# Kernel optimization log

Measured on AMD Instinct MI355X. Metric: run time of the kernel, lower is better.

Reference implementation:

```python
import jax, jax.numpy as jnp
import numpy as np

B, R, N, D_IN, D_OUT = 8, 8, 1024, 256, 256


def setup_inputs() -> dict:
    key = jax.random.key(0)
    k1, k2, k3, k4 = jax.random.split(key, 4)
    x = jax.random.normal(k1, (B, N, D_IN), dtype=jnp.float32)
    adj_stack = jax.random.uniform(k2, (B, R, N, N), dtype=jnp.float32)
    # per-relation Linear params, stacked: W[r] maps D_IN -> D_OUT
    bound = 1.0 / np.sqrt(D_IN)
    W = jax.random.uniform(k3, (R, D_IN, D_OUT), minval=-bound, maxval=bound, dtype=jnp.float32)
    b = jax.random.uniform(k4, (R, D_OUT), minval=-bound, maxval=bound, dtype=jnp.float32)
    return {"x": x, "adj_stack": adj_stack, "W": W, "b": b}


def reference(x, adj_stack, W, b):
    # support[b,r,n,e] = x[b,n,:] @ W[r] + b[r]
    support = jnp.einsum('bnd,rde->brne', x, W) + b[None, :, None, :]
    # out[b,m,e] = sum_r adj[b,r,m,:] @ support[b,r,:,e]
    out = jnp.einsum('brmn,brne->bme', adj_stack, support)
    return jax.nn.relu(out)
```

## Files before the change

### kernel.cpp

```cpp
#include <hip/hip_runtime.h>


#define Rr 8
#define Nn 1024
#define Dd 256
#define SP 104
#define EPF 68
#define EPS 72

typedef __attribute__((ext_vector_type(8))) short short8;
typedef __attribute__((ext_vector_type(4))) float f32x4;

__device__ __forceinline__ short f2bf(float f) {
    unsigned u = __builtin_bit_cast(unsigned, f);
    u += 0x7fffu + ((u >> 16) & 1u);
    return (short)(u >> 16);
}

__device__ __forceinline__ short8 cvt8(f32x4 lo, f32x4 hi) {
    short8 t;
    t[0] = f2bf(lo[0]); t[1] = f2bf(lo[1]); t[2] = f2bf(lo[2]); t[3] = f2bf(lo[3]);
    t[4] = f2bf(hi[0]); t[5] = f2bf(hi[1]); t[6] = f2bf(hi[2]); t[7] = f2bf(hi[3]);
    return t;
}

__global__ void prep_w_kernel(const float* __restrict__ W, short* __restrict__ Wt) {
    __shared__ short T[64][72];
    const int tid = threadIdx.x;
    const int et = blockIdx.x, dt = blockIdx.y, r = blockIdx.z;
    const float* Wr = W + ((size_t)r * Dd + dt * 64) * Dd + et * 64;
    #pragma unroll
    for (int i = 0; i < 4; ++i) {
        int idx = tid + i * 256;
        int d_l = idx >> 4;
        int e4  = (idx & 15) * 4;
        f32x4 v = *(const f32x4*)(Wr + d_l * Dd + e4);
        T[e4 + 0][d_l] = f2bf(v[0]);
        T[e4 + 1][d_l] = f2bf(v[1]);
        T[e4 + 2][d_l] = f2bf(v[2]);
        T[e4 + 3][d_l] = f2bf(v[3]);
    }
    __syncthreads();
    short* o = Wt + ((size_t)r * Dd + et * 64) * Dd + dt * 64;
    #pragma unroll
    for (int i = 0; i < 2; ++i) {
        int idx = tid + i * 256;
        *(short8*)(o + (idx >> 3) * Dd + (idx & 7) * 8) = *(const short8*)&T[idx >> 3][(idx & 7) * 8];
    }
}

__global__ __launch_bounds__(256, 3) void support_kernel(
        const float* __restrict__ x, const short* __restrict__ Wt,
        const float* __restrict__ bias, short* __restrict__ sup) {
    __shared__ short As[2][64 * SP];
    __shared__ short Bs[2][64 * SP];

    const int tid = threadIdx.x;
    const int wave = tid >> 6, lane = tid & 63;
    const int quad = lane >> 4, l16 = lane & 15;
    const int lrow = tid >> 3, lc = tid & 7;
    const int d = blockIdx.x;
    const int b = d & 7, rest = d >> 3;
    const int e_t = rest & 3, n_t = (rest >> 2) & 15, r = rest >> 6;
    const int e0 = e_t * 64, n0 = n_t * 64;
    const int we = wave & 1, wn = wave >> 1;

    const short* wp = Wt + ((size_t)r * Dd + e0) * Dd;
    const float* xb = x + ((size_t)b * Nn + n0) * Dd;

    short8 Wa0[2], Wa1[2];
    f32x4  Xv0[4], Xv1[4];

#define SGLOAD(WW, XX, t) do { int d0_ = (t) * 64;                              \
        _Pragma("unroll")                                                       \
        for (int p_ = 0; p_ < 2; ++p_) { int row_ = lrow + p_ * 32;             \
            WW[p_] = *(const short8*)(wp + (size_t)row_ * Dd + d0_ + lc * 8);   \
            const float* px_ = xb + (size_t)row_ * Dd + d0_ + lc * 8;           \
            XX[2 * p_]     = *(const f32x4*)px_;                                \
            XX[2 * p_ + 1] = *(const f32x4*)(px_ + 4); } } while (0)

#define SWRITE(BW, WW, XX) do {                                                 \
        _Pragma("unroll")                                                       \
        for (int p_ = 0; p_ < 2; ++p_) { int row_ = lrow + p_ * 32;             \
            *(short8*)&As[BW][row_ * SP + lc * 8] = WW[p_];                     \
            *(short8*)&Bs[BW][row_ * SP + lc * 8] = cvt8(XX[2 * p_], XX[2 * p_ + 1]); } } while (0)

#define SCOMP(BR) do {                                                          \
        _Pragma("unroll")                                                       \
        for (int kk_ = 0; kk_ < 2; ++kk_) { short8 af_[2], bf_[2];              \
            _Pragma("unroll")                                                   \
            for (int i_ = 0; i_ < 2; ++i_)                                      \
                af_[i_] = *(const short8*)&As[BR][(we * 32 + i_ * 16 + l16) * SP + kk_ * 32 + quad * 8]; \
            _Pragma("unroll")                                                   \
            for (int j_ = 0; j_ < 2; ++j_)                                      \
                bf_[j_] = *(const short8*)&Bs[BR][(wn * 32 + j_ * 16 + l16) * SP + kk_ * 32 + quad * 8]; \
            __builtin_amdgcn_s_setprio(1);                                      \
            _Pragma("unroll")                                                   \
            for (int i_ = 0; i_ < 2; ++i_)                                      \
                _Pragma("unroll")                                               \
                for (int j_ = 0; j_ < 2; ++j_)                                  \
                    acc[i_][j_] = __builtin_amdgcn_mfma_f32_16x16x32_bf16(af_[i_], bf_[j_], acc[i_][j_], 0, 0, 0); \
            __builtin_amdgcn_s_setprio(0); } } while (0)

#define SITER(t, VM, BW, WW, XX, BR) do {                                       \
        asm volatile("s_waitcnt vmcnt(" #VM ")" ::: "memory");                  \
        asm volatile("s_waitcnt lgkmcnt(0)" ::: "memory");                      \
        __builtin_amdgcn_s_barrier();                                           \
        asm volatile("" ::: "memory");                                          \
        SWRITE(BW, WW, XX);                                                     \
        if ((t) + 3 < 4) SGLOAD(WW, XX, (t) + 3);                               \
        SCOMP(BR); } while (0)

    f32x4 acc[2][2] = {};
    SGLOAD(Wa0, Xv0, 0);
    SGLOAD(Wa1, Xv1, 1);
    asm volatile("s_waitcnt vmcnt(6)" ::: "memory");
    SWRITE(0, Wa0, Xv0);
    SGLOAD(Wa0, Xv0, 2);
    SITER(0, 6, 1, Wa1, Xv1, 0);
    SITER(1, 6, 0, Wa0, Xv0, 1);
    SITER(2, 0, 1, Wa1, Xv1, 0);
    asm volatile("s_waitcnt lgkmcnt(0)" ::: "memory");
    __builtin_amdgcn_s_barrier();
    asm volatile("" ::: "memory");
    SCOMP(1);
#undef SGLOAD
#undef SWRITE
#undef SCOMP
#undef SITER

    __syncthreads();
    short* E = &As[0][0];
    #pragma unroll
    for (int i = 0; i < 2; ++i)
        #pragma unroll
        for (int reg = 0; reg < 4; ++reg) {
            int e_l = we * 32 + i * 16 + quad * 4 + reg;
            float bv = bias[r * Dd + e0 + e_l];
            #pragma unroll
            for (int j = 0; j < 2; ++j)
                E[e_l * EPS + wn * 32 + j * 16 + l16] = f2bf(acc[i][j][reg] + bv);
        }
    __syncthreads();
    #pragma unroll
    for (int p = 0; p < 2; ++p) {
        int idx = tid + p * 256;
        int row = idx >> 3, c = idx & 7;
        *(short8*)(sup + (((size_t)((b * Rr + r) * Dd + e0 + row)) << 10) + n0 + c * 8) =
            *(const short8*)&E[row * EPS + c * 8];
    }
}

__global__ __launch_bounds__(256, 3) void gcn_gemm_kernel(
        const float* __restrict__ adj, const short* __restrict__ sup,
        float* __restrict__ out) {
    __shared__ short As[2][64 * SP];
    __shared__ short Bs[2][64 * SP];

    const int tid = threadIdx.x;
    const int wave = tid >> 6, lane = tid & 63;
    const int quad = lane >> 4, l16 = lane & 15;
    const int lrow = tid >> 3, lc = tid & 7;
    const int d = blockIdx.x;
    const int L = (d & 7) * 64 + (d >> 3);
    const int e_t = L & 3, mrow = L >> 2;
    const int b = mrow >> 4;
    const int m0 = (mrow & 15) * 64, e0 = e_t * 64;
    const int wm = wave & 1, we = wave >> 1;

    f32x4  Aa0[4], Aa1[4];
    short8 Sv0[2], Sv1[2];

#define GGLOAD(AA, SS, t) do { int r_ = (t) >> 4, n0_ = ((t) & 15) * 64;        \
        const float* ap_ = adj + ((size_t)((b * Rr + r_) * Nn + m0)) * Nn + n0_; \
        const short* sp_ = sup + (((size_t)((b * Rr + r_) * Dd + e0)) << 10) + n0_; \
        _Pragma("unroll")                                                       \
        for (int p_ = 0; p_ < 2; ++p_) { int row_ = lrow + p_ * 32;             \
            const float* pa_ = ap_ + (size_t)row_ * Nn + lc * 8;                \
            AA[2 * p_]     = *(const f32x4*)pa_;                                \
            AA[2 * p_ + 1] = *(const f32x4*)(pa_ + 4);                          \
            SS[p_] = *(const short8*)(sp_ + ((size_t)row_ << 10) + lc * 8); } } while (0)

#define GWRITE(BW, AA, SS) do {                                                 \
        _Pragma("unroll")                                                       \
        for (int p_ = 0; p_ < 2; ++p_) { int row_ = lrow + p_ * 32;             \
            *(short8*)&As[BW][row_ * SP + lc * 8] = cvt8(AA[2 * p_], AA[2 * p_ + 1]); \
            *(short8*)&Bs[BW][row_ * SP + lc * 8] = SS[p_]; } } while (0)

#define GCOMP(BR) do {                                                          \
        _Pragma("unroll")                                                       \
        for (int kk_ = 0; kk_ < 2; ++kk_) { short8 af_[2], bf_[2];              \
            _Pragma("unroll")                                                   \
            for (int i_ = 0; i_ < 2; ++i_)                                      \
                af_[i_] = *(const short8*)&As[BR][(wm * 32 + i_ * 16 + l16) * SP + kk_ * 32 + quad * 8]; \
            _Pragma("unroll")                                                   \
            for (int j_ = 0; j_ < 2; ++j_)                                      \
                bf_[j_] = *(const short8*)&Bs[BR][(we * 32 + j_ * 16 + l16) * SP + kk_ * 32 + quad * 8]; \
            __builtin_amdgcn_s_setprio(1);                                      \
            _Pragma("unroll")                                                   \
            for (int i_ = 0; i_ < 2; ++i_)                                      \
                _Pragma("unroll")                                               \
                for (int j_ = 0; j_ < 2; ++j_)                                  \
                    acc[i_][j_] = __builtin_amdgcn_mfma_f32_16x16x32_bf16(af_[i_], bf_[j_], acc[i_][j_], 0, 0, 0); \
            __builtin_amdgcn_s_setprio(0); } } while (0)

#define GITER(t, VM, BW, AA, SS, BR) do {                                       \
        asm volatile("s_waitcnt vmcnt(" #VM ")" ::: "memory");                  \
        asm volatile("s_waitcnt lgkmcnt(0)" ::: "memory");                      \
        __builtin_amdgcn_s_barrier();                                           \
        asm volatile("" ::: "memory");                                          \
        GWRITE(BW, AA, SS);                                                     \
        if ((t) + 3 < 128) GGLOAD(AA, SS, (t) + 3);                             \
        GCOMP(BR); } while (0)

    f32x4 acc[2][2] = {};
    GGLOAD(Aa0, Sv0, 0);
    GGLOAD(Aa1, Sv1, 1);
    asm volatile("s_waitcnt vmcnt(6)" ::: "memory");
    GWRITE(0, Aa0, Sv0);
    GGLOAD(Aa0, Sv0, 2);
    for (int t = 0; t < 126; t += 2) {
        GITER(t,     6, 1, Aa1, Sv1, 0);
        GITER(t + 1, 6, 0, Aa0, Sv0, 1);
    }
    GITER(126, 0, 1, Aa1, Sv1, 0);
    asm volatile("s_waitcnt lgkmcnt(0)" ::: "memory");
    __builtin_amdgcn_s_barrier();
    asm volatile("" ::: "memory");
    GCOMP(1);
#undef GGLOAD
#undef GWRITE
#undef GCOMP
#undef GITER

    __syncthreads();
    float* E = (float*)&As[0][0];
    #pragma unroll
    for (int i = 0; i < 2; ++i)
        #pragma unroll
        for (int reg = 0; reg < 4; ++reg) {
            int m_l = wm * 32 + i * 16 + quad * 4 + reg;
            #pragma unroll
            for (int j = 0; j < 2; ++j)
                E[m_l * EPF + we * 32 + j * 16 + l16] = fmaxf(acc[i][j][reg], 0.f);
        }
    __syncthreads();
    #pragma unroll
    for (int p = 0; p < 4; ++p) {
        int idx = tid + p * 256;
        int row = idx >> 4, c = idx & 15;
        *(f32x4*)(out + ((size_t)(b * Nn + m0 + row)) * Dd + e0 + c * 4) =
            *(const f32x4*)&E[row * EPF + c * 4];
    }
}

extern "C" void kernel_launch(void* const* d_in, const int* in_sizes, int n_in,
                              void* d_out, int out_size, void* d_ws, size_t ws_size,
                              hipStream_t stream) {
    const float* x    = (const float*)d_in[0];
    const float* adj  = (const float*)d_in[1];
    const float* W    = (const float*)d_in[2];
    const float* bias = (const float*)d_in[3];
    float* out = (float*)d_out;
    short* sup = (short*)d_ws;
    short* Wt  = (short*)((char*)d_ws + (32u << 20));

    prep_w_kernel<<<dim3(4, 4, 8), 256, 0, stream>>>(W, Wt);
    support_kernel<<<4096, 256, 0, stream>>>(x, Wt, bias, sup);
    gcn_gemm_kernel<<<512, 256, 0, stream>>>(adj, sup, out);
}
```

Measured before the change: 442.3 us.

## Pre-pack support in MFMA fragment layout and load it directly into registers

The support kernel now writes its bf16 output in a packed layout that matches the MFMA B-operand fragment order, so the main GEMM loads B fragments straight from global memory into registers and skips LDS for them. The main GEMM tile changes from 64x64 to 32x128 (m by e), and only the adjacency tile is staged in LDS, through a 4-deep buffer with one barrier per iteration. This is meant to cut LDS traffic and barrier count in the bandwidth-bound adjacency stream. In exchange it holds more register buffers and issues uncoalesced-looking per-wave B loads from L2.

```diff
diff --git a/kernel.cpp b/kernel.cpp
--- a/kernel.cpp
+++ b/kernel.cpp
@@ -4,11 +4,12 @@
 #define Rr 8
 #define Nn 1024
 #define Dd 256
-#define SP 104
-#define EPF 68
+#define AP 104
+#define EP2 132
 #define EPS 72
 
 typedef __attribute__((ext_vector_type(8))) short short8;
+typedef __attribute__((ext_vector_type(4))) short short4s;
 typedef __attribute__((ext_vector_type(4))) float f32x4;
 
 __device__ __forceinline__ short f2bf(float f) {
@@ -21,6 +22,12 @@
     short8 t;
     t[0] = f2bf(lo[0]); t[1] = f2bf(lo[1]); t[2] = f2bf(lo[2]); t[3] = f2bf(lo[3]);
     t[4] = f2bf(hi[0]); t[5] = f2bf(hi[1]); t[6] = f2bf(hi[2]); t[7] = f2bf(hi[3]);
+    return t;
+}
+
+__device__ __forceinline__ short4s cvt4(f32x4 v) {
+    short4s t;
+    t[0] = f2bf(v[0]); t[1] = f2bf(v[1]); t[2] = f2bf(v[2]); t[3] = f2bf(v[3]);
     return t;
 }
 
@@ -51,9 +58,9 @@
 
 __global__ __launch_bounds__(256, 3) void support_kernel(
         const float* __restrict__ x, const short* __restrict__ Wt,
-        const float* __restrict__ bias, short* __restrict__ sup) {
-    __shared__ short As[2][64 * SP];
-    __shared__ short Bs[2][64 * SP];
+        const float* __restrict__ bias, short* __restrict__ supP) {
+    __shared__ short As[2][64 * AP];
+    __shared__ short Bs[2][64 * AP];
 
     const int tid = threadIdx.x;
     const int wave = tid >> 6, lane = tid & 63;
@@ -82,18 +89,18 @@
 #define SWRITE(BW, WW, XX) do {                                                 \
         _Pragma("unroll")                                                       \
         for (int p_ = 0; p_ < 2; ++p_) { int row_ = lrow + p_ * 32;             \
-            *(short8*)&As[BW][row_ * SP + lc * 8] = WW[p_];                     \
-            *(short8*)&Bs[BW][row_ * SP + lc * 8] = cvt8(XX[2 * p_], XX[2 * p_ + 1]); } } while (0)
+            *(short8*)&As[BW][row_ * AP + lc * 8] = WW[p_];                     \
+            *(short8*)&Bs[BW][row_ * AP + lc * 8] = cvt8(XX[2 * p_], XX[2 * p_ + 1]); } } while (0)
 
 #define SCOMP(BR) do {                                                          \
         _Pragma("unroll")                                                       \
         for (int kk_ = 0; kk_ < 2; ++kk_) { short8 af_[2], bf_[2];              \
             _Pragma("unroll")                                                   \
             for (int i_ = 0; i_ < 2; ++i_)                                      \
-                af_[i_] = *(const short8*)&As[BR][(we * 32 + i_ * 16 + l16) * SP + kk_ * 32 + quad * 8]; \
+                af_[i_] = *(const short8*)&As[BR][(we * 32 + i_ * 16 + l16) * AP + kk_ * 32 + quad * 8]; \
             _Pragma("unroll")                                                   \
             for (int j_ = 0; j_ < 2; ++j_)                                      \
-                bf_[j_] = *(const short8*)&Bs[BR][(wn * 32 + j_ * 16 + l16) * SP + kk_ * 32 + quad * 8]; \
+                bf_[j_] = *(const short8*)&Bs[BR][(wn * 32 + j_ * 16 + l16) * AP + kk_ * 32 + quad * 8]; \
             __builtin_amdgcn_s_setprio(1);                                      \
             _Pragma("unroll")                                                   \
             for (int i_ = 0; i_ < 2; ++i_)                                      \
@@ -144,113 +151,116 @@
     __syncthreads();
     #pragma unroll
     for (int p = 0; p < 2; ++p) {
-        int idx = tid + p * 256;
-        int row = idx >> 3, c = idx & 7;
-        *(short8*)(sup + (((size_t)((b * Rr + r) * Dd + e0 + row)) << 10) + n0 + c * 8) =
-            *(const short8*)&E[row * EPS + c * 8];
+        int chunk = tid + p * 256;
+        int e_l = chunk & 63, n8 = chunk >> 6;
+        int e_g = e0 + e_l;
+        int pet = e_g >> 7, pwv = (e_g >> 5) & 3, pj = (e_g >> 4) & 1, pl = e_g & 15;
+        int kh = n8 >> 2, qd = n8 & 3;
+        size_t off = ((((((size_t)((b * Rr + r) * 16 + n_t) * 2 + pet) * 4 + pwv) * 2 + pj) * 2 + kh) * 64
+                      + (qd * 16 + pl)) * 8;
+        *(short8*)(supP + off) = *(const short8*)&E[e_l * EPS + n8 * 8];
     }
 }
 
 __global__ __launch_bounds__(256, 3) void gcn_gemm_kernel(
-        const float* __restrict__ adj, const short* __restrict__ sup,
+        const float* __restrict__ adj, const short* __restrict__ supP,
         float* __restrict__ out) {
-    __shared__ short As[2][64 * SP];
-    __shared__ short Bs[2][64 * SP];
+    __shared__ short AsL[4][32 * AP];
 
     const int tid = threadIdx.x;
-    const int wave = tid >> 6, lane = tid & 63;
+    const int wv = tid >> 6, lane = tid & 63;
     const int quad = lane >> 4, l16 = lane & 15;
-    const int lrow = tid >> 3, lc = tid & 7;
     const int d = blockIdx.x;
-    const int L = (d & 7) * 64 + (d >> 3);
-    const int e_t = L & 3, mrow = L >> 2;
-    const int b = mrow >> 4;
-    const int m0 = (mrow & 15) * 64, e0 = e_t * 64;
-    const int wm = wave & 1, we = wave >> 1;
-
-    f32x4  Aa0[4], Aa1[4];
-    short8 Sv0[2], Sv1[2];
-
-#define GGLOAD(AA, SS, t) do { int r_ = (t) >> 4, n0_ = ((t) & 15) * 64;        \
+    const int b = d & 7, z = d >> 3;
+    const int et = z & 1, m0 = (z >> 1) * 32;
+    const int arow = tid >> 4, ac4 = (tid & 15) * 4;
+
+    f32x4  Aa0[2], Aa1[2];
+    short8 Sv0[4], Sv1[4], Sv2[4], Sv3[4];
+    f32x4  acc[2][2] = {};
+
+#define GADJ(AA, t) do { int r_ = (t) >> 4, n0_ = ((t) & 15) * 64;              \
         const float* ap_ = adj + ((size_t)((b * Rr + r_) * Nn + m0)) * Nn + n0_; \
-        const short* sp_ = sup + (((size_t)((b * Rr + r_) * Dd + e0)) << 10) + n0_; \
-        _Pragma("unroll")                                                       \
-        for (int p_ = 0; p_ < 2; ++p_) { int row_ = lrow + p_ * 32;             \
-            const float* pa_ = ap_ + (size_t)row_ * Nn + lc * 8;                \
-            AA[2 * p_]     = *(const f32x4*)pa_;                                \
-            AA[2 * p_ + 1] = *(const f32x4*)(pa_ + 4);                          \
-            SS[p_] = *(const short8*)(sp_ + ((size_t)row_ << 10) + lc * 8); } } while (0)
-
-#define GWRITE(BW, AA, SS) do {                                                 \
-        _Pragma("unroll")                                                       \
-        for (int p_ = 0; p_ < 2; ++p_) { int row_ = lrow + p_ * 32;             \
-            *(short8*)&As[BW][row_ * SP + lc * 8] = cvt8(AA[2 * p_], AA[2 * p_ + 1]); \
-            *(short8*)&Bs[BW][row_ * SP + lc * 8] = SS[p_]; } } while (0)
-
-#define GCOMP(BR) do {                                                          \
-        _Pragma("unroll")                                                       \
-        for (int kk_ = 0; kk_ < 2; ++kk_) { short8 af_[2], bf_[2];              \
-            _Pragma("unroll")                                                   \
-            for (int i_ = 0; i_ < 2; ++i_)                                      \
-                af_[i_] = *(const short8*)&As[BR][(wm * 32 + i_ * 16 + l16) * SP + kk_ * 32 + quad * 8]; \
-            _Pragma("unroll")                                                   \
-            for (int j_ = 0; j_ < 2; ++j_)                                      \
-                bf_[j_] = *(const short8*)&Bs[BR][(we * 32 + j_ * 16 + l16) * SP + kk_ * 32 + quad * 8]; \
-            __builtin_amdgcn_s_setprio(1);                                      \
+        AA[0] = *(const f32x4*)(ap_ + (size_t)arow * Nn + ac4);                 \
+        AA[1] = *(const f32x4*)(ap_ + (size_t)(arow + 16) * Nn + ac4); } while (0)
+
+#define GSUP(SS, t) do { int r_ = (t) >> 4, ns_ = (t) & 15;                     \
+        const short* sp_ = supP + ((((size_t)(b * Rr + r_) * 16 + ns_) * 2 + et) * 4 + wv) * 2048 + lane * 8; \
+        SS[0] = *(const short8*)(sp_);                                          \
+        SS[1] = *(const short8*)(sp_ + 512);                                    \
+        SS[2] = *(const short8*)(sp_ + 1024);                                   \
+        SS[3] = *(const short8*)(sp_ + 1536); } while (0)
+
+#define GWRITE(BW, AA) do {                                                     \
+        *(short4s*)&AsL[BW][arow * AP + ac4] = cvt4(AA[0]);                     \
+        *(short4s*)&AsL[BW][(arow + 16) * AP + ac4] = cvt4(AA[1]); } while (0)
+
+#define GCOMP(SS, BR) do { short8 af_[4];                                       \
+        _Pragma("unroll")                                                       \
+        for (int i_ = 0; i_ < 2; ++i_)                                          \
+            _Pragma("unroll")                                                   \
+            for (int kh_ = 0; kh_ < 2; ++kh_)                                   \
+                af_[i_ * 2 + kh_] = *(const short8*)&AsL[BR][(i_ * 16 + l16) * AP + kh_ * 32 + quad * 8]; \
+        asm volatile("s_waitcnt lgkmcnt(0)" ::: "memory");                      \
+        __builtin_amdgcn_sched_barrier(0);                                      \
+        __builtin_amdgcn_s_setprio(1);                                          \
+        _Pragma("unroll")                                                       \
+        for (int kh_ = 0; kh_ < 2; ++kh_)                                       \
             _Pragma("unroll")                                                   \
             for (int i_ = 0; i_ < 2; ++i_)                                      \
                 _Pragma("unroll")                                               \
                 for (int j_ = 0; j_ < 2; ++j_)                                  \
-                    acc[i_][j_] = __builtin_amdgcn_mfma_f32_16x16x32_bf16(af_[i_], bf_[j_], acc[i_][j_], 0, 0, 0); \
-            __builtin_amdgcn_s_setprio(0); } } while (0)
-
-#define GITER(t, VM, BW, AA, SS, BR) do {                                       \
+                    acc[i_][j_] = __builtin_amdgcn_mfma_f32_16x16x32_bf16(af_[i_ * 2 + kh_], SS[j_ * 2 + kh_], acc[i_][j_], 0, 0, 0); \
+        __builtin_amdgcn_s_setprio(0); } while (0)
+
+#define GITER(t, VM, SR, SW, AW, BW, BR, DOI, DOW) do {                         \
         asm volatile("s_waitcnt vmcnt(" #VM ")" ::: "memory");                  \
-        asm volatile("s_waitcnt lgkmcnt(0)" ::: "memory");                      \
+        if (DOW) GWRITE(BW, AW);                                                \
+        if (DOI) { GADJ(AW, (t) + 3); GSUP(SW, (t) + 3); }                      \
+        GCOMP(SR, BR);                                                          \
         __builtin_amdgcn_s_barrier();                                           \
-        asm volatile("" ::: "memory");                                          \
-        GWRITE(BW, AA, SS);                                                     \
-        if ((t) + 3 < 128) GGLOAD(AA, SS, (t) + 3);                             \
-        GCOMP(BR); } while (0)
-
-    f32x4 acc[2][2] = {};
-    GGLOAD(Aa0, Sv0, 0);
-    GGLOAD(Aa1, Sv1, 1);
-    asm volatile("s_waitcnt vmcnt(6)" ::: "memory");
-    GWRITE(0, Aa0, Sv0);
-    GGLOAD(Aa0, Sv0, 2);
-    for (int t = 0; t < 126; t += 2) {
-        GITER(t,     6, 1, Aa1, Sv1, 0);
-        GITER(t + 1, 6, 0, Aa0, Sv0, 1);
-    }
-    GITER(126, 0, 1, Aa1, Sv1, 0);
+        asm volatile("" ::: "memory"); } while (0)
+
+    GADJ(Aa0, 0); GSUP(Sv0, 0);
+    GADJ(Aa1, 1); GSUP(Sv1, 1);
+    asm volatile("s_waitcnt vmcnt(10)" ::: "memory");
+    GWRITE(0, Aa0);
+    GADJ(Aa0, 2); GSUP(Sv2, 2);
     asm volatile("s_waitcnt lgkmcnt(0)" ::: "memory");
     __builtin_amdgcn_s_barrier();
     asm volatile("" ::: "memory");
-    GCOMP(1);
-#undef GGLOAD
+
+    for (int t0 = 0; t0 < 124; t0 += 4) {
+        GITER(t0 + 0, 10, Sv0, Sv3, Aa1, 1, 0, 1, 1);
+        GITER(t0 + 1, 10, Sv1, Sv0, Aa0, 2, 1, 1, 1);
+        GITER(t0 + 2, 10, Sv2, Sv1, Aa1, 3, 2, 1, 1);
+        GITER(t0 + 3, 10, Sv3, Sv2, Aa0, 0, 3, 1, 1);
+    }
+    GITER(124, 10, Sv0, Sv3, Aa1, 1, 0, 1, 1);
+    GITER(125, 10, Sv1, Sv0, Aa0, 2, 1, 0, 1);
+    GITER(126, 4,  Sv2, Sv1, Aa1, 3, 2, 0, 1);
+    GITER(127, 0,  Sv3, Sv2, Aa0, 0, 3, 0, 0);
+#undef GADJ
+#undef GSUP
 #undef GWRITE
 #undef GCOMP
 #undef GITER
 
-    __syncthreads();
-    float* E = (float*)&As[0][0];
+    float* E = (float*)&AsL[0][0];
     #pragma unroll
     for (int i = 0; i < 2; ++i)
         #pragma unroll
-        for (int reg = 0; reg < 4; ++reg) {
-            int m_l = wm * 32 + i * 16 + quad * 4 + reg;
+        for (int j = 0; j < 2; ++j)
             #pragma unroll
-            for (int j = 0; j < 2; ++j)
-                E[m_l * EPF + we * 32 + j * 16 + l16] = fmaxf(acc[i][j][reg], 0.f);
-        }
-    __syncthreads();
-    #pragma unroll
-    for (int p = 0; p < 4; ++p) {
-        int idx = tid + p * 256;
-        int row = idx >> 4, c = idx & 15;
-        *(f32x4*)(out + ((size_t)(b * Nn + m0 + row)) * Dd + e0 + c * 4) =
-            *(const f32x4*)&E[row * EPF + c * 4];
+            for (int reg = 0; reg < 4; ++reg)
+                E[(i * 16 + quad * 4 + reg) * EP2 + wv * 32 + j * 16 + l16] =
+                    fmaxf(acc[i][j][reg], 0.f);
+    __syncthreads();
+    float* ob = out + ((size_t)(b * Nn + m0)) * Dd + et * 128;
+    #pragma unroll
+    for (int k = 0; k < 4; ++k) {
+        int row = tid >> 3, c = (tid & 7) * 16 + k * 4;
+        *(f32x4*)(ob + (size_t)row * Dd + c) = *(const f32x4*)&E[row * EP2 + c];
     }
 }
 
@@ -262,10 +272,10 @@
     const float* W    = (const float*)d_in[2];
     const float* bias = (const float*)d_in[3];
     float* out = (float*)d_out;
-    short* sup = (short*)d_ws;
-    short* Wt  = (short*)((char*)d_ws + (32u << 20));
+    short* supP = (short*)d_ws;
+    short* Wt   = (short*)((char*)d_ws + (40u << 20));
 
     prep_w_kernel<<<dim3(4, 4, 8), 256, 0, stream>>>(W, Wt);
-    support_kernel<<<4096, 256, 0, stream>>>(x, Wt, bias, sup);
-    gcn_gemm_kernel<<<512, 256, 0, stream>>>(adj, sup, out);
-}
+    support_kernel<<<4096, 256, 0, stream>>>(x, Wt, bias, supP);
+    gcn_gemm_kernel<<<512, 256, 0, stream>>>(adj, supP, out);
+}
```

New measurement: 443.0 us. About the same (+0.2%).
